# Kernel optimization log

Hardware: AMD Instinct MI355X
Metric: run time of the kernel (lower is better)

## Reference

```python
import jax, jax.numpy as jnp
import numpy as np

T = 64      # simulation_length
B = 128     # batch
D = 2048    # flattened input dim / axons per core
N = 2048    # neurons per core
L = 4       # number of cores (chain, latency = index)
OUT = 1024  # number of output_sources


def setup_inputs() -> dict:
    key = jax.random.key(0)
    k0, k1, k2, k3 = jax.random.split(key, 4)
    x = jax.random.uniform(k0, (B, D), dtype=jnp.float32)          # rate-coded input in [0,1)
    # core_params[l] = core_matrix.transpose() -> shape [N, A]; scaled for sane membrane dynamics
    W = jax.random.normal(k1, (L, N, D), dtype=jnp.float32) * 0.05
    thresholds = jnp.ones((L,), dtype=jnp.float32)
    # axon_sources: per-core irregular gather indices into previous core's neurons (input for l=0)
    axon_idx = jax.random.randint(k2, (L, D), 0, D, dtype=jnp.int32)
    out_idx = jax.random.randint(k3, (OUT,), 0, N, dtype=jnp.int32)
    return dict(x=x, W=W, thresholds=thresholds, axon_idx=axon_idx,
                out_idx=out_idx, simulation_length=T)


def _ideal_spike_scan(avg, thr, T):
    """Per-cycle: m += avg; spike = (m > thr); m[m > thr] -= thr.  avg: [B, N]."""
    def step(m, _):
        m = m + avg
        s = (m > thr).astype(m.dtype)
        return m - thr * s, s
    _, spikes = jax.lax.scan(step, jnp.zeros_like(avg), None, length=T)
    return spikes  # [T, B, N]


def reference(x, W, thresholds, axon_idx, out_idx, simulation_length):
    T = simulation_length
    L = W.shape[0]
    # generate_input_spike_train: x replicated across all cycles -> cache[-1]
    prev = jnp.broadcast_to(x, (T,) + x.shape)  # [T, B, D]
    for l in range(L):
        # get_signal_tensor: gather axon source signals for every cycle
        gathered = prev[:, :, axon_idx[l]]                    # [T, B, A]
        # per-cycle matmul: torch.matmul(core_params, sig.T).T == sig @ W[l].T
        val = jnp.einsum('tba,na->tbn', gathered, W[l])       # [T, B, N]
        avg = val.mean(axis=0)                                # avg_values [B, N]
        # ideal membrane integrate + threshold-reset recurrence -> out spike train
        prev = _ideal_spike_scan(avg, thresholds[l], T)       # [T, B, N]
    # output_signals: sum of output-source spikes over all cycles
    return prev[:, :, out_idx].sum(axis=0)                    # [B, OUT]
```

## Files before the change

kernel.cpp:

```cpp
#include <hip/hip_runtime.h>

#define BB   128
#define DD   2048
#define NN   2048
#define LL   4
#define OUTN 1024
#define JBQ  32
#define NDIG 5

#define NWDIG 12288
#define NG0   1024
#define NCSR  4

typedef double double4v __attribute__((ext_vector_type(4)));
typedef int    int4v    __attribute__((ext_vector_type(4)));
typedef char   char4v   __attribute__((ext_vector_type(4)));

__global__ __launch_bounds__(256) void prep_kernel(
    const float* __restrict__ W1,
    const float* __restrict__ x,
    const int*   __restrict__ axon,
    const int*   __restrict__ oidx,
    signed char* __restrict__ Wd,
    float*       __restrict__ At,
    int*         __restrict__ off,
    int*         __restrict__ lst)
{
    __shared__ int hist[2048];
    __shared__ int part[256];

    const int t  = threadIdx.x;
    const int bk = blockIdx.x;
    const size_t DP = (size_t)NN * DD;

    if (bk < NWDIG) {
        size_t i  = (size_t)bk * 256 + t;
        int    l  = (int)(i / (DP / 4));
        size_t e4 = i - (size_t)l * (DP / 4);
        int n = (int)(e4 >> 9);
        int k = (int)(e4 & 511) * 4;
        float4 w = *(const float4*)(W1 + (size_t)l * DP + (size_t)n * DD + k);
        const float wv[4] = {w.x, w.y, w.z, w.w};
        unsigned long long V[4];
        #pragma unroll
        for (int e = 0; e < 4; ++e)
            V[e] = (unsigned long long)(__double2ll_rn((double)wv[e] * 0x1p33)
                                        + (1LL << 34));
        signed char* base = Wd + (size_t)l * 5 * DP
                          + (size_t)(n >> 5) * 65536 + (size_t)(k >> 6) * 2048
                          + (n & 31) * 64 + (k & 63);
        #pragma unroll
        for (int j = 0; j < NDIG; ++j) {
            char4v p = { (char)((V[0] >> (7 * j)) & 127),
                         (char)((V[1] >> (7 * j)) & 127),
                         (char)((V[2] >> (7 * j)) & 127),
                         (char)((V[3] >> (7 * j)) & 127) };
            *(char4v*)(base + (size_t)j * DP) = p;
        }
        return;
    }
    if (bk < NWDIG + NG0) {
        int i = (bk - NWDIG) * 256 + t;
        int k = i >> 7;
        int b = i & 127;
        At[i] = x[b * DD + axon[k]];
        return;
    }
    {
        const int m   = bk - (NWDIG + NG0);
        const int* ip = (m < 3) ? (axon + (size_t)(m + 1) * DD) : oidx;
        const int cnt = (m < 3) ? DD : OUTN;
        int* offG = off + m * 2052;
        int* lstG = lst + m * 2048;

        for (int i = t; i < 2048; i += 256) hist[i] = 0;
        __syncthreads();
        for (int e = t; e < cnt; e += 256) atomicAdd(&hist[ip[e]], 1);
        __syncthreads();

        const int b0 = t * 8;
        int s = 0;
        #pragma unroll
        for (int i = 0; i < 8; ++i) s += hist[b0 + i];
        part[t] = s;
        __syncthreads();
        for (int d = 1; d < 256; d <<= 1) {
            int v = (t >= d) ? part[t - d] : 0;
            __syncthreads();
            part[t] += v;
            __syncthreads();
        }
        int base = part[t] - s;
        #pragma unroll
        for (int i = 0; i < 8; ++i) {
            int h = hist[b0 + i];
            offG[b0 + i] = base;
            hist[b0 + i] = base;
            base += h;
        }
        if (t == 255) offG[2048] = base;
        __syncthreads();
        for (int e = t; e < cnt; e += 256) {
            int n = ip[e];
            int pos = atomicAdd(&hist[n], 1);
            lstG[pos] = e;
        }
    }
}

__global__ __launch_bounds__(256, 2) void layer_kernel(
    const float* __restrict__ src,
    const int*   __restrict__ idx,
    int sR, int sB,
    const float* __restrict__ Wl,
    const float* __restrict__ thresholds, int l,
    const int*   __restrict__ Tptr,
    float* __restrict__ dst,
    const int* __restrict__ goff, const int* __restrict__ glst,
    signed char* __restrict__ g8n,
    const int* __restrict__ ooff, const int* __restrict__ olst,
    float* __restrict__ outp,
    int isLast)
{
    __shared__ double red[4 * 64 * 8];

    const int t    = threadIdx.x;
    const int wq   = t >> 6;
    const int lane = t & 63;
    const int q    = lane >> 4;
    const int c    = lane & 15;

    const int g     = blockIdx.x;
    const int btile = (g >> 3) & 7;
    const int nsup  = (g & 7) | ((g >> 6) << 3);
    const int n0    = nsup * 32;
    const int bcol  = btile * 16 + c;
    const size_t bo = (size_t)bcol * sB;

    double4v pr = {0., 0., 0., 0.}, pcv = {0., 0., 0., 0.};
    pr  = __builtin_amdgcn_mfma_f64_16x16x4f64(0.25 * (double)c, 1.0, pr, 0, 0, 0);
    pcv = __builtin_amdgcn_mfma_f64_16x16x4f64(0.25, (double)c, pcv, 0, 0, 0);
    int rowD[4], colD[4];
    #pragma unroll
    for (int r = 0; r < 4; ++r) {
        rowD[r] = (int)(pr[r] + 0.25);
        colD[r] = (int)(pcv[r] + 0.25);
    }

    double4v acc0[4] = {{0.,0.,0.,0.},{0.,0.,0.,0.},{0.,0.,0.,0.},{0.,0.,0.,0.}};
    double4v acc1[4] = {{0.,0.,0.,0.},{0.,0.,0.,0.},{0.,0.,0.,0.},{0.,0.,0.,0.}};

    const int    kbase = wq * (DD / 4);
    const float* wb0   = Wl + (size_t)(n0 + c) * DD + kbase + 4 * q;
    const float* wb1   = wb0 + (size_t)16 * DD;
    const int*   ibase = idx ? (idx + kbase + 4 * q) : nullptr;

    float4 wv0[4], wv1[4];
    float4 sv[4];
    int4   iv[4];

    #pragma unroll
    for (int p = 0; p < 4; ++p) {
        wv0[p] = *(const float4*)(wb0 + 16 * p);
        wv1[p] = *(const float4*)(wb1 + 16 * p);
    }
    #pragma unroll
    for (int p = 0; p < 4; ++p) {
        int r0, r1, r2, r3;
        if (ibase) {
            int4 iv0 = *(const int4*)(ibase + 16 * p);
            r0 = iv0.x; r1 = iv0.y; r2 = iv0.z; r3 = iv0.w;
        } else {
            int kb = kbase + 16 * p + 4 * q;
            r0 = kb; r1 = kb + 1; r2 = kb + 2; r3 = kb + 3;
        }
        sv[p].x = src[(size_t)r0 * sR + bo];
        sv[p].y = src[(size_t)r1 * sR + bo];
        sv[p].z = src[(size_t)r2 * sR + bo];
        sv[p].w = src[(size_t)r3 * sR + bo];
    }
    if (ibase) {
        #pragma unroll
        for (int p = 0; p < 4; ++p) iv[p] = *(const int4*)(ibase + 16 * (4 + p));
    }

    for (int u = 0; u < JBQ / 4; ++u) {
        #pragma unroll
        for (int gg = 0; gg < 4; ++gg) {
            float4 w0 = wv0[gg];
            float4 w1 = wv1[gg];
            float4 s  = sv[gg];

            int jn = 4 * u + 4 + gg; if (jn > JBQ - 1) jn = JBQ - 1;
            wv0[gg] = *(const float4*)(wb0 + 16 * jn);
            wv1[gg] = *(const float4*)(wb1 + 16 * jn);

            int r0, r1, r2, r3;
            if (ibase) {
                int4 ivv = iv[gg];
                r0 = ivv.x; r1 = ivv.y; r2 = ivv.z; r3 = ivv.w;
            } else {
                int kb = kbase + 16 * jn + 4 * q;
                r0 = kb; r1 = kb + 1; r2 = kb + 2; r3 = kb + 3;
            }
            sv[gg].x = src[(size_t)r0 * sR + bo];
            sv[gg].y = src[(size_t)r1 * sR + bo];
            sv[gg].z = src[(size_t)r2 * sR + bo];
            sv[gg].w = src[(size_t)r3 * sR + bo];

            if (ibase) {
                int jm = 4 * u + 8 + gg; if (jm > JBQ - 1) jm = JBQ - 1;
                iv[gg] = *(const int4*)(ibase + 16 * jm);
            }

            acc0[0] = __builtin_amdgcn_mfma_f64_16x16x4f64((double)w0.x, (double)s.x, acc0[0], 0, 0, 0);
            acc1[0] = __builtin_amdgcn_mfma_f64_16x16x4f64((double)w1.x, (double)s.x, acc1[0], 0, 0, 0);
            acc0[1] = __builtin_amdgcn_mfma_f64_16x16x4f64((double)w0.y, (double)s.y, acc0[1], 0, 0, 0);
            acc1[1] = __builtin_amdgcn_mfma_f64_16x16x4f64((double)w1.y, (double)s.y, acc1[1], 0, 0, 0);
            acc0[2] = __builtin_amdgcn_mfma_f64_16x16x4f64((double)w0.z, (double)s.z, acc0[2], 0, 0, 0);
            acc1[2] = __builtin_amdgcn_mfma_f64_16x16x4f64((double)w1.z, (double)s.z, acc1[2], 0, 0, 0);
            acc0[3] = __builtin_amdgcn_mfma_f64_16x16x4f64((double)w0.w, (double)s.w, acc0[3], 0, 0, 0);
            acc1[3] = __builtin_amdgcn_mfma_f64_16x16x4f64((double)w1.w, (double)s.w, acc1[3], 0, 0, 0);
        }
    }

    double4v a0 = (acc0[0] + acc0[1]) + (acc0[2] + acc0[3]);
    double4v a1 = (acc1[0] + acc1[1]) + (acc1[2] + acc1[3]);

    {
        double* my = red + ((size_t)wq * 64 + lane) * 8;
        #pragma unroll
        for (int r = 0; r < 4; ++r) { my[r] = a0[r]; my[4 + r] = a1[r]; }
    }
    __syncthreads();
    if (wq < 2) {
        const int off = wq * 4;
        double a[4];
        #pragma unroll
        for (int r = 0; r < 4; ++r) {
            a[r] =  red[((size_t)0 * 64 + lane) * 8 + off + r];
            a[r] += red[((size_t)1 * 64 + lane) * 8 + off + r];
            a[r] += red[((size_t)2 * 64 + lane) * 8 + off + r];
            a[r] += red[((size_t)3 * 64 + lane) * 8 + off + r];
        }

        const double th = (double)thresholds[l];
        const int T = *Tptr;
        const float sc = isLast ? 1.0f : (1.0f / (float)T);
        double m0 = 0., m1 = 0., m2 = 0., m3 = 0.;
        int c0 = 0, c1 = 0, c2 = 0, c3 = 0;
        for (int tt = 0; tt < T; ++tt) {
            m0 += a[0]; if (m0 > th) { c0++; m0 -= th; }
            m1 += a[1]; if (m1 > th) { c1++; m1 -= th; }
            m2 += a[2]; if (m2 > th) { c2++; m2 -= th; }
            m3 += a[3]; if (m3 > th) { c3++; m3 -= th; }
        }
        int cnt[4] = {c0, c1, c2, c3};
        #pragma unroll
        for (int r = 0; r < 4; ++r) {
            int n = n0 + 16 * wq + rowD[r];
            int b = btile * 16 + colD[r];
            if (dst)  dst[(size_t)n * BB + b] = (float)cnt[r] * sc;
            if (goff) {
                for (int j = goff[n]; j < goff[n + 1]; ++j) {
                    int k = glst[j];
                    g8n[(size_t)(k >> 6) * 8192 + b * 64 + (k & 63)] =
                        (signed char)cnt[r];
                }
            }
            if (ooff) {
                for (int j = ooff[n]; j < ooff[n + 1]; ++j)
                    outp[(size_t)b * OUTN + olst[j]] = (float)cnt[r];
            }
        }
    }
}

__global__ __launch_bounds__(256, 2) void layer_i8_kernel(
    const signed char* __restrict__ B8,
    const signed char* __restrict__ Wd5,
    const float* __restrict__ thresholds, int l,
    const int*   __restrict__ Tptr,
    const int* __restrict__ goff, const int* __restrict__ glst,
    signed char* __restrict__ g8n,
    const int* __restrict__ ooff, const int* __restrict__ olst,
    float* __restrict__ outp,
    int isLast)
{
    __shared__ double red[4 * 64 * 8];

    const int t    = threadIdx.x;
    const int wq   = t >> 6;
    const int lane = t & 63;
    const int q    = lane >> 4;
    const int c    = lane & 15;

    const int g     = blockIdx.x;
    const int btile = (g >> 3) & 7;
    const int nsup  = (g & 7) | ((g >> 6) << 3);
    const int n0    = nsup * 32;
    const int bcol  = btile * 16 + c;

    int rowD[4], colD[4];
    {
        const int cb  = c * 0x01010101;
        const int hot = (q == 0) ? 1 : 0;
        int4v aLab = {cb, cb, cb, cb};
        int4v oneh = {hot, 0, 0, 0};
        int4v dR = {0, 0, 0, 0}, dC = {0, 0, 0, 0};
        dR = __builtin_amdgcn_mfma_i32_16x16x64_i8(aLab, oneh, dR, 0, 0, 0);
        dC = __builtin_amdgcn_mfma_i32_16x16x64_i8(oneh, aLab, dC, 0, 0, 0);
        #pragma unroll
        for (int r = 0; r < 4; ++r) { rowD[r] = dR[r]; colD[r] = dC[r]; }
    }

    int4v acc0[NDIG], acc1[NDIG], accS = (int4v)0;
    #pragma unroll
    for (int j = 0; j < NDIG; ++j) { acc0[j] = (int4v)0; acc1[j] = (int4v)0; }

    const size_t DP = (size_t)NN * DD;
    const signed char* ab = Wd5 + (size_t)nsup * 65536 + c * 64 + q * 16;
    const signed char* bb = B8 + bcol * 64 + q * 16;

    const int4v ones = {0x01010101, 0x01010101, 0x01010101, 0x01010101};
    const int ck0 = wq * 8;

    int4v A0[NDIG], A1[NDIG], Bv;
    int4v N0[NDIG], N1[NDIG], Nb;

    {
        const signed char* ap = ab + (size_t)ck0 * 2048;
        #pragma unroll
        for (int j = 0; j < NDIG; ++j) {
            A0[j] = *(const int4v*)(ap + (size_t)j * DP);
            A1[j] = *(const int4v*)(ap + (size_t)j * DP + 1024);
        }
        Bv = *(const int4v*)(bb + (size_t)ck0 * 8192);
    }

    #pragma unroll 1
    for (int u = 0; u < 3; ++u) {
        {
            const signed char* ap = ab + (size_t)(ck0 + 2 * u + 1) * 2048;
            #pragma unroll
            for (int j = 0; j < NDIG; ++j) {
                N0[j] = *(const int4v*)(ap + (size_t)j * DP);
                N1[j] = *(const int4v*)(ap + (size_t)j * DP + 1024);
            }
            Nb = *(const int4v*)(bb + (size_t)(ck0 + 2 * u + 1) * 8192);
        }
        #pragma unroll
        for (int j = 0; j < NDIG; ++j) {
            acc0[j] = __builtin_amdgcn_mfma_i32_16x16x64_i8(A0[j], Bv, acc0[j], 0, 0, 0);
            acc1[j] = __builtin_amdgcn_mfma_i32_16x16x64_i8(A1[j], Bv, acc1[j], 0, 0, 0);
        }
        accS = __builtin_amdgcn_mfma_i32_16x16x64_i8(ones, Bv, accS, 0, 0, 0);
        {
            const signed char* ap = ab + (size_t)(ck0 + 2 * u + 2) * 2048;
            #pragma unroll
            for (int j = 0; j < NDIG; ++j) {
                A0[j] = *(const int4v*)(ap + (size_t)j * DP);
                A1[j] = *(const int4v*)(ap + (size_t)j * DP + 1024);
            }
            Bv = *(const int4v*)(bb + (size_t)(ck0 + 2 * u + 2) * 8192);
        }
        #pragma unroll
        for (int j = 0; j < NDIG; ++j) {
            acc0[j] = __builtin_amdgcn_mfma_i32_16x16x64_i8(N0[j], Nb, acc0[j], 0, 0, 0);
            acc1[j] = __builtin_amdgcn_mfma_i32_16x16x64_i8(N1[j], Nb, acc1[j], 0, 0, 0);
        }
        accS = __builtin_amdgcn_mfma_i32_16x16x64_i8(ones, Nb, accS, 0, 0, 0);
    }
    {
        const signed char* ap = ab + (size_t)(ck0 + 7) * 2048;
        #pragma unroll
        for (int j = 0; j < NDIG; ++j) {
            N0[j] = *(const int4v*)(ap + (size_t)j * DP);
            N1[j] = *(const int4v*)(ap + (size_t)j * DP + 1024);
        }
        Nb = *(const int4v*)(bb + (size_t)(ck0 + 7) * 8192);
    }
    #pragma unroll
    for (int j = 0; j < NDIG; ++j) {
        acc0[j] = __builtin_amdgcn_mfma_i32_16x16x64_i8(A0[j], Bv, acc0[j], 0, 0, 0);
        acc1[j] = __builtin_amdgcn_mfma_i32_16x16x64_i8(A1[j], Bv, acc1[j], 0, 0, 0);
    }
    accS = __builtin_amdgcn_mfma_i32_16x16x64_i8(ones, Bv, accS, 0, 0, 0);
    #pragma unroll
    for (int j = 0; j < NDIG; ++j) {
        acc0[j] = __builtin_amdgcn_mfma_i32_16x16x64_i8(N0[j], Nb, acc0[j], 0, 0, 0);
        acc1[j] = __builtin_amdgcn_mfma_i32_16x16x64_i8(N1[j], Nb, acc1[j], 0, 0, 0);
    }
    accS = __builtin_amdgcn_mfma_i32_16x16x64_i8(ones, Nb, accS, 0, 0, 0);

    const double S0 = 0x1p-33, S1 = 0x1p-26, S2 = 0x1p-19,
                 S3 = 0x1p-12, S4 = 0x1p-5;
    {
        double* my = red + ((size_t)wq * 64 + lane) * 8;
        #pragma unroll
        for (int r = 0; r < 4; ++r) {
            double corr = 2.0 * (double)accS[r];
            my[r]     = S0 * (double)acc0[0][r] + S1 * (double)acc0[1][r]
                      + S2 * (double)acc0[2][r] + S3 * (double)acc0[3][r]
                      + S4 * (double)acc0[4][r] - corr;
            my[4 + r] = S0 * (double)acc1[0][r] + S1 * (double)acc1[1][r]
                      + S2 * (double)acc1[2][r] + S3 * (double)acc1[3][r]
                      + S4 * (double)acc1[4][r] - corr;
        }
    }
    __syncthreads();
    if (wq < 2) {
        const int off = wq * 4;
        double a[4];
        #pragma unroll
        for (int r = 0; r < 4; ++r) {
            a[r] =  red[((size_t)0 * 64 + lane) * 8 + off + r];
            a[r] += red[((size_t)1 * 64 + lane) * 8 + off + r];
            a[r] += red[((size_t)2 * 64 + lane) * 8 + off + r];
            a[r] += red[((size_t)3 * 64 + lane) * 8 + off + r];
        }

        const double th = (double)thresholds[l];
        const int T = *Tptr;
        const double invT = 1.0 / (double)T;
        double m0 = 0., m1 = 0., m2 = 0., m3 = 0.;
        int c0 = 0, c1 = 0, c2 = 0, c3 = 0;
        const double v0 = a[0] * invT, v1 = a[1] * invT,
                     v2 = a[2] * invT, v3 = a[3] * invT;
        for (int tt = 0; tt < T; ++tt) {
            m0 += v0; if (m0 > th) { c0++; m0 -= th; }
            m1 += v1; if (m1 > th) { c1++; m1 -= th; }
            m2 += v2; if (m2 > th) { c2++; m2 -= th; }
            m3 += v3; if (m3 > th) { c3++; m3 -= th; }
        }
        int cnt[4] = {c0, c1, c2, c3};
        #pragma unroll
        for (int r = 0; r < 4; ++r) {
            int n = n0 + 16 * wq + rowD[r];
            int b = btile * 16 + colD[r];
            if (goff) {
                for (int j = goff[n]; j < goff[n + 1]; ++j) {
                    int k = glst[j];
                    g8n[(size_t)(k >> 6) * 8192 + b * 64 + (k & 63)] =
                        (signed char)cnt[r];
                }
            }
            if (ooff) {
                for (int j = ooff[n]; j < ooff[n + 1]; ++j)
                    outp[(size_t)b * OUTN + olst[j]] = (float)cnt[r];
            }
        }
    }
}

__global__ __launch_bounds__(256) void out_kernel(
    const float* __restrict__ cntT, const int* __restrict__ out_idx,
    float* __restrict__ out)
{
    int i = blockIdx.x * 256 + threadIdx.x;
    int b = i >> 10;
    int o = i & 1023;
    out[i] = cntT[(size_t)out_idx[o] * BB + b];
}

extern "C" void kernel_launch(void* const* d_in, const int* in_sizes, int n_in,
                              void* d_out, int out_size, void* d_ws, size_t ws_size,
                              hipStream_t stream)
{
    const float* x    = (const float*)d_in[0];
    const float* W    = (const float*)d_in[1];
    const float* thr  = (const float*)d_in[2];
    const int*   axon = (const int*)d_in[3];
    const int*   oidx = (const int*)d_in[4];
    const int*   Tptr = (const int*)d_in[5];
    float* out = (float*)d_out;

    const size_t DP = (size_t)NN * DD;
    char* ws = (char*)d_ws;
    float* At   = (float*)ws;
    float* mA   = (float*)(ws + (1u << 20));
    float* mB   = (float*)(ws + (2u << 20));
    float* cntT = (float*)(ws + (3u << 20));
    signed char* g8A = (signed char*)(ws + (4u << 20));
    signed char* g8B = (signed char*)(ws + (4u << 20) + (256u << 10));
    int* off = (int*)(ws + (4u << 20) + (512u << 10));
    int* lst = (int*)(ws + (4u << 20) + (640u << 10));
    signed char* Wd  = (signed char*)(ws + (5u << 20));

    const int useI8 = (ws_size >= ((size_t)80 << 20)) ? 1 : 0;

    if (!useI8) {
        const float* srcs[LL] = { x, mA, mB, mA };
        float*       dsts[LL] = { mA, mB, mA, cntT };
        for (int l = 0; l < LL; ++l) {
            layer_kernel<<<512, 256, 0, stream>>>(
                srcs[l], axon + (size_t)l * DD,
                (l == 0) ? 1 : BB, (l == 0) ? DD : 1,
                W + (size_t)l * NN * DD, thr, l, Tptr,
                dsts[l], nullptr, nullptr, nullptr, nullptr, nullptr, nullptr,
                (l == LL - 1) ? 1 : 0);
        }
        out_kernel<<<(BB * OUTN) / 256, 256, 0, stream>>>(cntT, oidx, out);
        return;
    }

    prep_kernel<<<NWDIG + NG0 + NCSR, 256, 0, stream>>>(
        W + DP, x, axon, oidx, Wd, At, off, lst);

    layer_kernel<<<512, 256, 0, stream>>>(
        At, nullptr, BB, 1, W, thr, 0, Tptr,
        nullptr, off + 0 * 2052, lst + 0 * 2048, g8A,
        nullptr, nullptr, nullptr, 0);

    layer_i8_kernel<<<512, 256, 0, stream>>>(
        g8A, Wd + 0 * 5 * DP, thr, 1, Tptr,
        off + 1 * 2052, lst + 1 * 2048, g8B,
        nullptr, nullptr, nullptr, 0);
    layer_i8_kernel<<<512, 256, 0, stream>>>(
        g8B, Wd + 1 * 5 * DP, thr, 2, Tptr,
        off + 2 * 2052, lst + 2 * 2048, g8A,
        nullptr, nullptr, nullptr, 0);
    layer_i8_kernel<<<512, 256, 0, stream>>>(
        g8A, Wd + 2 * 5 * DP, thr, 3, Tptr,
        nullptr, nullptr, nullptr,
        off + 3 * 2052, lst + 3 * 2048, out, 1);
}
```

Before: 215.1 us.

## Halve neuron tile per block and double grid for layer kernels, retile layer-0 input

Layer-0 now runs in a dedicated kernel with a 16-neuron tile, and its gathered input is stored in a k-chunked tiled layout that matches the int8 buffers. The int8 layer kernels also drop from 32 to 16 neurons per block, with the grid doubled to 1024 blocks and launch bounds raised to 4 blocks per CU. The aim is more parallelism and occupancy on the many CUs. In exchange, the software-pipelined double-buffered prefetch in the int8 kernel becomes a simple load-then-MFMA loop, and each block reuses its B operand over fewer neurons.

```diff
diff --git a/kernel.cpp b/kernel.cpp
--- a/kernel.cpp
+++ b/kernel.cpp
@@ -61,9 +61,9 @@
     }
     if (bk < NWDIG + NG0) {
         int i = (bk - NWDIG) * 256 + t;
-        int k = i >> 7;
-        int b = i & 127;
-        At[i] = x[b * DD + axon[k]];
+        int b = i >> 11;
+        int k = i & (DD - 1);
+        At[(size_t)(k >> 6) * 8192 + b * 64 + (k & 63)] = x[b * DD + axon[k]];
         return;
     }
     {
@@ -108,6 +108,231 @@
     }
 }
 
+__global__ __launch_bounds__(256, 4) void layer0_kernel(
+    const float* __restrict__ Atile,
+    const float* __restrict__ Wl,
+    const float* __restrict__ thr,
+    const int*   __restrict__ Tptr,
+    const int* __restrict__ goff, const int* __restrict__ glst,
+    signed char* __restrict__ g8n)
+{
+    __shared__ double red[4 * 64 * 4];
+
+    const int t    = threadIdx.x;
+    const int wq   = t >> 6;
+    const int lane = t & 63;
+    const int q    = lane >> 4;
+    const int c    = lane & 15;
+
+    const int g     = blockIdx.x;
+    const int btile = (g >> 3) & 7;
+    const int nsup  = (g & 7) | ((g >> 6) << 3);
+    const int n0    = nsup * 16;
+    const int bcol  = btile * 16 + c;
+
+    double4v pr = {0., 0., 0., 0.}, pcv = {0., 0., 0., 0.};
+    pr  = __builtin_amdgcn_mfma_f64_16x16x4f64(0.25 * (double)c, 1.0, pr, 0, 0, 0);
+    pcv = __builtin_amdgcn_mfma_f64_16x16x4f64(0.25, (double)c, pcv, 0, 0, 0);
+    int rowD[4], colD[4];
+    #pragma unroll
+    for (int r = 0; r < 4; ++r) {
+        rowD[r] = (int)(pr[r] + 0.25);
+        colD[r] = (int)(pcv[r] + 0.25);
+    }
+
+    double4v acc[4] = {{0.,0.,0.,0.},{0.,0.,0.,0.},{0.,0.,0.,0.},{0.,0.,0.,0.}};
+
+    const int    kbase = wq * (DD / 4);
+    const float* wb0   = Wl + (size_t)(n0 + c) * DD + kbase + 4 * q;
+
+    float4 wv0[4], sv[4];
+    #pragma unroll
+    for (int p = 0; p < 4; ++p) wv0[p] = *(const float4*)(wb0 + 16 * p);
+    #pragma unroll
+    for (int p = 0; p < 4; ++p) {
+        int kabs = kbase + 16 * p + 4 * q;
+        sv[p] = *(const float4*)(Atile + (size_t)(kabs >> 6) * 8192
+                                 + bcol * 64 + (kabs & 63));
+    }
+
+    for (int u = 0; u < JBQ / 4; ++u) {
+        #pragma unroll
+        for (int gg = 0; gg < 4; ++gg) {
+            float4 w0 = wv0[gg];
+            float4 s  = sv[gg];
+
+            int jn = 4 * u + 4 + gg; if (jn > JBQ - 1) jn = JBQ - 1;
+            wv0[gg] = *(const float4*)(wb0 + 16 * jn);
+            int kabs = kbase + 16 * jn + 4 * q;
+            sv[gg] = *(const float4*)(Atile + (size_t)(kabs >> 6) * 8192
+                                      + bcol * 64 + (kabs & 63));
+
+            acc[0] = __builtin_amdgcn_mfma_f64_16x16x4f64((double)w0.x, (double)s.x, acc[0], 0, 0, 0);
+            acc[1] = __builtin_amdgcn_mfma_f64_16x16x4f64((double)w0.y, (double)s.y, acc[1], 0, 0, 0);
+            acc[2] = __builtin_amdgcn_mfma_f64_16x16x4f64((double)w0.z, (double)s.z, acc[2], 0, 0, 0);
+            acc[3] = __builtin_amdgcn_mfma_f64_16x16x4f64((double)w0.w, (double)s.w, acc[3], 0, 0, 0);
+        }
+    }
+
+    double4v a0 = (acc[0] + acc[1]) + (acc[2] + acc[3]);
+    {
+        double* my = red + ((size_t)wq * 64 + lane) * 4;
+        #pragma unroll
+        for (int r = 0; r < 4; ++r) my[r] = a0[r];
+    }
+    __syncthreads();
+    if (wq == 0) {
+        double a[4];
+        #pragma unroll
+        for (int r = 0; r < 4; ++r) {
+            a[r] =  red[((size_t)0 * 64 + lane) * 4 + r];
+            a[r] += red[((size_t)1 * 64 + lane) * 4 + r];
+            a[r] += red[((size_t)2 * 64 + lane) * 4 + r];
+            a[r] += red[((size_t)3 * 64 + lane) * 4 + r];
+        }
+
+        const double th = (double)thr[0];
+        const int T = *Tptr;
+        double m0 = 0., m1 = 0., m2 = 0., m3 = 0.;
+        int c0 = 0, c1 = 0, c2 = 0, c3 = 0;
+        for (int tt = 0; tt < T; ++tt) {
+            m0 += a[0]; if (m0 > th) { c0++; m0 -= th; }
+            m1 += a[1]; if (m1 > th) { c1++; m1 -= th; }
+            m2 += a[2]; if (m2 > th) { c2++; m2 -= th; }
+            m3 += a[3]; if (m3 > th) { c3++; m3 -= th; }
+        }
+        int cnt[4] = {c0, c1, c2, c3};
+        #pragma unroll
+        for (int r = 0; r < 4; ++r) {
+            int n = n0 + rowD[r];
+            int b = btile * 16 + colD[r];
+            for (int j = goff[n]; j < goff[n + 1]; ++j) {
+                int k = glst[j];
+                g8n[(size_t)(k >> 6) * 8192 + b * 64 + (k & 63)] =
+                    (signed char)cnt[r];
+            }
+        }
+    }
+}
+
+__global__ __launch_bounds__(256, 4) void layer_i8_kernel(
+    const signed char* __restrict__ B8,
+    const signed char* __restrict__ Wd5,
+    const float* __restrict__ thr, int l,
+    const int*   __restrict__ Tptr,
+    const int* __restrict__ goff, const int* __restrict__ glst,
+    signed char* __restrict__ g8n,
+    const int* __restrict__ ooff, const int* __restrict__ olst,
+    float* __restrict__ outp)
+{
+    __shared__ double red[4 * 64 * 4];
+
+    const int t    = threadIdx.x;
+    const int wq   = t >> 6;
+    const int lane = t & 63;
+    const int q    = lane >> 4;
+    const int c    = lane & 15;
+
+    const int g     = blockIdx.x;
+    const int btile = (g >> 3) & 7;
+    const int nsup  = (g & 7) | ((g >> 6) << 3);
+    const int n0    = nsup * 16;
+    const int bcol  = btile * 16 + c;
+
+    int rowD[4], colD[4];
+    {
+        const int cb  = c * 0x01010101;
+        const int hot = (q == 0) ? 1 : 0;
+        int4v aLab = {cb, cb, cb, cb};
+        int4v oneh = {hot, 0, 0, 0};
+        int4v dR = {0, 0, 0, 0}, dC = {0, 0, 0, 0};
+        dR = __builtin_amdgcn_mfma_i32_16x16x64_i8(aLab, oneh, dR, 0, 0, 0);
+        dC = __builtin_amdgcn_mfma_i32_16x16x64_i8(oneh, aLab, dC, 0, 0, 0);
+        #pragma unroll
+        for (int r = 0; r < 4; ++r) { rowD[r] = dR[r]; colD[r] = dC[r]; }
+    }
+
+    int4v acc[NDIG], accS = (int4v)0;
+    #pragma unroll
+    for (int j = 0; j < NDIG; ++j) acc[j] = (int4v)0;
+
+    const size_t DP = (size_t)NN * DD;
+    const signed char* ab = Wd5 + (size_t)(nsup >> 1) * 65536
+                          + (nsup & 1) * 1024 + c * 64 + q * 16;
+    const signed char* bb = B8 + bcol * 64 + q * 16;
+
+    const int4v ones = {0x01010101, 0x01010101, 0x01010101, 0x01010101};
+    const int ck0 = wq * 8;
+
+    #pragma unroll 1
+    for (int kc = 0; kc < 8; ++kc) {
+        const signed char* ap = ab + (size_t)(ck0 + kc) * 2048;
+        int4v A[NDIG], Bv;
+        #pragma unroll
+        for (int j = 0; j < NDIG; ++j)
+            A[j] = *(const int4v*)(ap + (size_t)j * DP);
+        Bv = *(const int4v*)(bb + (size_t)(ck0 + kc) * 8192);
+        #pragma unroll
+        for (int j = 0; j < NDIG; ++j)
+            acc[j] = __builtin_amdgcn_mfma_i32_16x16x64_i8(A[j], Bv, acc[j], 0, 0, 0);
+        accS = __builtin_amdgcn_mfma_i32_16x16x64_i8(ones, Bv, accS, 0, 0, 0);
+    }
+
+    const double S0 = 0x1p-33, S1 = 0x1p-26, S2 = 0x1p-19,
+                 S3 = 0x1p-12, S4 = 0x1p-5;
+    {
+        double* my = red + ((size_t)wq * 64 + lane) * 4;
+        #pragma unroll
+        for (int r = 0; r < 4; ++r) {
+            my[r] = S0 * (double)acc[0][r] + S1 * (double)acc[1][r]
+                  + S2 * (double)acc[2][r] + S3 * (double)acc[3][r]
+                  + S4 * (double)acc[4][r] - 2.0 * (double)accS[r];
+        }
+    }
+    __syncthreads();
+    if (wq == 0) {
+        double a[4];
+        #pragma unroll
+        for (int r = 0; r < 4; ++r) {
+            a[r] =  red[((size_t)0 * 64 + lane) * 4 + r];
+            a[r] += red[((size_t)1 * 64 + lane) * 4 + r];
+            a[r] += red[((size_t)2 * 64 + lane) * 4 + r];
+            a[r] += red[((size_t)3 * 64 + lane) * 4 + r];
+        }
+
+        const double th = (double)thr[l];
+        const int T = *Tptr;
+        const double invT = 1.0 / (double)T;
+        double m0 = 0., m1 = 0., m2 = 0., m3 = 0.;
+        int c0 = 0, c1 = 0, c2 = 0, c3 = 0;
+        const double v0 = a[0] * invT, v1 = a[1] * invT,
+                     v2 = a[2] * invT, v3 = a[3] * invT;
+        for (int tt = 0; tt < T; ++tt) {
+            m0 += v0; if (m0 > th) { c0++; m0 -= th; }
+            m1 += v1; if (m1 > th) { c1++; m1 -= th; }
+            m2 += v2; if (m2 > th) { c2++; m2 -= th; }
+            m3 += v3; if (m3 > th) { c3++; m3 -= th; }
+        }
+        int cnt[4] = {c0, c1, c2, c3};
+        #pragma unroll
+        for (int r = 0; r < 4; ++r) {
+            int n = n0 + rowD[r];
+            int b = btile * 16 + colD[r];
+            if (goff) {
+                for (int j = goff[n]; j < goff[n + 1]; ++j) {
+                    int k = glst[j];
+                    g8n[(size_t)(k >> 6) * 8192 + b * 64 + (k & 63)] =
+                        (signed char)cnt[r];
+                }
+            }
+            if (ooff) {
+                for (int j = ooff[n]; j < ooff[n + 1]; ++j)
+                    outp[(size_t)b * OUTN + olst[j]] = (float)cnt[r];
+            }
+        }
+    }
+}
+
 __global__ __launch_bounds__(256, 2) void layer_kernel(
     const float* __restrict__ src,
     const int*   __restrict__ idx,
@@ -115,12 +340,7 @@
     const float* __restrict__ Wl,
     const float* __restrict__ thresholds, int l,
     const int*   __restrict__ Tptr,
-    float* __restrict__ dst,
-    const int* __restrict__ goff, const int* __restrict__ glst,
-    signed char* __restrict__ g8n,
-    const int* __restrict__ ooff, const int* __restrict__ olst,
-    float* __restrict__ outp,
-    int isLast)
+    float* __restrict__ dst, int isLast)
 {
     __shared__ double red[4 * 64 * 8];
 
@@ -260,195 +480,7 @@
         for (int r = 0; r < 4; ++r) {
             int n = n0 + 16 * wq + rowD[r];
             int b = btile * 16 + colD[r];
-            if (dst)  dst[(size_t)n * BB + b] = (float)cnt[r] * sc;
-            if (goff) {
-                for (int j = goff[n]; j < goff[n + 1]; ++j) {
-                    int k = glst[j];
-                    g8n[(size_t)(k >> 6) * 8192 + b * 64 + (k & 63)] =
-                        (signed char)cnt[r];
-                }
-            }
-            if (ooff) {
-                for (int j = ooff[n]; j < ooff[n + 1]; ++j)
-                    outp[(size_t)b * OUTN + olst[j]] = (float)cnt[r];
-            }
-        }
-    }
-}
-
-__global__ __launch_bounds__(256, 2) void layer_i8_kernel(
-    const signed char* __restrict__ B8,
-    const signed char* __restrict__ Wd5,
-    const float* __restrict__ thresholds, int l,
-    const int*   __restrict__ Tptr,
-    const int* __restrict__ goff, const int* __restrict__ glst,
-    signed char* __restrict__ g8n,
-    const int* __restrict__ ooff, const int* __restrict__ olst,
-    float* __restrict__ outp,
-    int isLast)
-{
-    __shared__ double red[4 * 64 * 8];
-
-    const int t    = threadIdx.x;
-    const int wq   = t >> 6;
-    const int lane = t & 63;
-    const int q    = lane >> 4;
-    const int c    = lane & 15;
-
-    const int g     = blockIdx.x;
-    const int btile = (g >> 3) & 7;
-    const int nsup  = (g & 7) | ((g >> 6) << 3);
-    const int n0    = nsup * 32;
-    const int bcol  = btile * 16 + c;
-
-    int rowD[4], colD[4];
-    {
-        const int cb  = c * 0x01010101;
-        const int hot = (q == 0) ? 1 : 0;
-        int4v aLab = {cb, cb, cb, cb};
-        int4v oneh = {hot, 0, 0, 0};
-        int4v dR = {0, 0, 0, 0}, dC = {0, 0, 0, 0};
-        dR = __builtin_amdgcn_mfma_i32_16x16x64_i8(aLab, oneh, dR, 0, 0, 0);
-        dC = __builtin_amdgcn_mfma_i32_16x16x64_i8(oneh, aLab, dC, 0, 0, 0);
-        #pragma unroll
-        for (int r = 0; r < 4; ++r) { rowD[r] = dR[r]; colD[r] = dC[r]; }
-    }
-
-    int4v acc0[NDIG], acc1[NDIG], accS = (int4v)0;
-    #pragma unroll
-    for (int j = 0; j < NDIG; ++j) { acc0[j] = (int4v)0; acc1[j] = (int4v)0; }
-
-    const size_t DP = (size_t)NN * DD;
-    const signed char* ab = Wd5 + (size_t)nsup * 65536 + c * 64 + q * 16;
-    const signed char* bb = B8 + bcol * 64 + q * 16;
-
-    const int4v ones = {0x01010101, 0x01010101, 0x01010101, 0x01010101};
-    const int ck0 = wq * 8;
-
-    int4v A0[NDIG], A1[NDIG], Bv;
-    int4v N0[NDIG], N1[NDIG], Nb;
-
-    {
-        const signed char* ap = ab + (size_t)ck0 * 2048;
-        #pragma unroll
-        for (int j = 0; j < NDIG; ++j) {
-            A0[j] = *(const int4v*)(ap + (size_t)j * DP);
-            A1[j] = *(const int4v*)(ap + (size_t)j * DP + 1024);
-        }
-        Bv = *(const int4v*)(bb + (size_t)ck0 * 8192);
-    }
-
-    #pragma unroll 1
-    for (int u = 0; u < 3; ++u) {
-        {
-            const signed char* ap = ab + (size_t)(ck0 + 2 * u + 1) * 2048;
-            #pragma unroll
-            for (int j = 0; j < NDIG; ++j) {
-                N0[j] = *(const int4v*)(ap + (size_t)j * DP);
-                N1[j] = *(const int4v*)(ap + (size_t)j * DP + 1024);
-            }
-            Nb = *(const int4v*)(bb + (size_t)(ck0 + 2 * u + 1) * 8192);
-        }
-        #pragma unroll
-        for (int j = 0; j < NDIG; ++j) {
-            acc0[j] = __builtin_amdgcn_mfma_i32_16x16x64_i8(A0[j], Bv, acc0[j], 0, 0, 0);
-            acc1[j] = __builtin_amdgcn_mfma_i32_16x16x64_i8(A1[j], Bv, acc1[j], 0, 0, 0);
-        }
-        accS = __builtin_amdgcn_mfma_i32_16x16x64_i8(ones, Bv, accS, 0, 0, 0);
-        {
-            const signed char* ap = ab + (size_t)(ck0 + 2 * u + 2) * 2048;
-            #pragma unroll
-            for (int j = 0; j < NDIG; ++j) {
-                A0[j] = *(const int4v*)(ap + (size_t)j * DP);
-                A1[j] = *(const int4v*)(ap + (size_t)j * DP + 1024);
-            }
-            Bv = *(const int4v*)(bb + (size_t)(ck0 + 2 * u + 2) * 8192);
-        }
-        #pragma unroll
-        for (int j = 0; j < NDIG; ++j) {
-            acc0[j] = __builtin_amdgcn_mfma_i32_16x16x64_i8(N0[j], Nb, acc0[j], 0, 0, 0);
-            acc1[j] = __builtin_amdgcn_mfma_i32_16x16x64_i8(N1[j], Nb, acc1[j], 0, 0, 0);
-        }
-        accS = __builtin_amdgcn_mfma_i32_16x16x64_i8(ones, Nb, accS, 0, 0, 0);
-    }
-    {
-        const signed char* ap = ab + (size_t)(ck0 + 7) * 2048;
-        #pragma unroll
-        for (int j = 0; j < NDIG; ++j) {
-            N0[j] = *(const int4v*)(ap + (size_t)j * DP);
-            N1[j] = *(const int4v*)(ap + (size_t)j * DP + 1024);
-        }
-        Nb = *(const int4v*)(bb + (size_t)(ck0 + 7) * 8192);
-    }
-    #pragma unroll
-    for (int j = 0; j < NDIG; ++j) {
-        acc0[j] = __builtin_amdgcn_mfma_i32_16x16x64_i8(A0[j], Bv, acc0[j], 0, 0, 0);
-        acc1[j] = __builtin_amdgcn_mfma_i32_16x16x64_i8(A1[j], Bv, acc1[j], 0, 0, 0);
-    }
-    accS = __builtin_amdgcn_mfma_i32_16x16x64_i8(ones, Bv, accS, 0, 0, 0);
-    #pragma unroll
-    for (int j = 0; j < NDIG; ++j) {
-        acc0[j] = __builtin_amdgcn_mfma_i32_16x16x64_i8(N0[j], Nb, acc0[j], 0, 0, 0);
-        acc1[j] = __builtin_amdgcn_mfma_i32_16x16x64_i8(N1[j], Nb, acc1[j], 0, 0, 0);
-    }
-    accS = __builtin_amdgcn_mfma_i32_16x16x64_i8(ones, Nb, accS, 0, 0, 0);
-
-    const double S0 = 0x1p-33, S1 = 0x1p-26, S2 = 0x1p-19,
-                 S3 = 0x1p-12, S4 = 0x1p-5;
-    {
-        double* my = red + ((size_t)wq * 64 + lane) * 8;
-        #pragma unroll
-        for (int r = 0; r < 4; ++r) {
-            double corr = 2.0 * (double)accS[r];
-            my[r]     = S0 * (double)acc0[0][r] + S1 * (double)acc0[1][r]
-                      + S2 * (double)acc0[2][r] + S3 * (double)acc0[3][r]
-                      + S4 * (double)acc0[4][r] - corr;
-            my[4 + r] = S0 * (double)acc1[0][r] + S1 * (double)acc1[1][r]
-                      + S2 * (double)acc1[2][r] + S3 * (double)acc1[3][r]
-                      + S4 * (double)acc1[4][r] - corr;
-        }
-    }
-    __syncthreads();
-    if (wq < 2) {
-        const int off = wq * 4;
-        double a[4];
-        #pragma unroll
-        for (int r = 0; r < 4; ++r) {
-            a[r] =  red[((size_t)0 * 64 + lane) * 8 + off + r];
-            a[r] += red[((size_t)1 * 64 + lane) * 8 + off + r];
-            a[r] += red[((size_t)2 * 64 + lane) * 8 + off + r];
-            a[r] += red[((size_t)3 * 64 + lane) * 8 + off + r];
-        }
-
-        const double th = (double)thresholds[l];
-        const int T = *Tptr;
-        const double invT = 1.0 / (double)T;
-        double m0 = 0., m1 = 0., m2 = 0., m3 = 0.;
-        int c0 = 0, c1 = 0, c2 = 0, c3 = 0;
-        const double v0 = a[0] * invT, v1 = a[1] * invT,
-                     v2 = a[2] * invT, v3 = a[3] * invT;
-        for (int tt = 0; tt < T; ++tt) {
-            m0 += v0; if (m0 > th) { c0++; m0 -= th; }
-            m1 += v1; if (m1 > th) { c1++; m1 -= th; }
-            m2 += v2; if (m2 > th) { c2++; m2 -= th; }
-            m3 += v3; if (m3 > th) { c3++; m3 -= th; }
-        }
-        int cnt[4] = {c0, c1, c2, c3};
-        #pragma unroll
-        for (int r = 0; r < 4; ++r) {
-            int n = n0 + 16 * wq + rowD[r];
-            int b = btile * 16 + colD[r];
-            if (goff) {
-                for (int j = goff[n]; j < goff[n + 1]; ++j) {
-                    int k = glst[j];
-                    g8n[(size_t)(k >> 6) * 8192 + b * 64 + (k & 63)] =
-                        (signed char)cnt[r];
-                }
-            }
-            if (ooff) {
-                for (int j = ooff[n]; j < ooff[n + 1]; ++j)
-                    outp[(size_t)b * OUTN + olst[j]] = (float)cnt[r];
-            }
+            dst[(size_t)n * BB + b] = (float)cnt[r] * sc;
         }
     }
 }
@@ -497,8 +529,7 @@
                 srcs[l], axon + (size_t)l * DD,
                 (l == 0) ? 1 : BB, (l == 0) ? DD : 1,
                 W + (size_t)l * NN * DD, thr, l, Tptr,
-                dsts[l], nullptr, nullptr, nullptr, nullptr, nullptr, nullptr,
-                (l == LL - 1) ? 1 : 0);
+                dsts[l], (l == LL - 1) ? 1 : 0);
         }
         out_kernel<<<(BB * OUTN) / 256, 256, 0, stream>>>(cntT, oidx, out);
         return;
@@ -507,21 +538,19 @@
     prep_kernel<<<NWDIG + NG0 + NCSR, 256, 0, stream>>>(
         W + DP, x, axon, oidx, Wd, At, off, lst);
 
-    layer_kernel<<<512, 256, 0, stream>>>(
-        At, nullptr, BB, 1, W, thr, 0, Tptr,
-        nullptr, off + 0 * 2052, lst + 0 * 2048, g8A,
-        nullptr, nullptr, nullptr, 0);
-
-    layer_i8_kernel<<<512, 256, 0, stream>>>(
+    layer0_kernel<<<1024, 256, 0, stream>>>(
+        At, W, thr, Tptr, off + 0 * 2052, lst + 0 * 2048, g8A);
+
+    layer_i8_kernel<<<1024, 256, 0, stream>>>(
         g8A, Wd + 0 * 5 * DP, thr, 1, Tptr,
         off + 1 * 2052, lst + 1 * 2048, g8B,
-        nullptr, nullptr, nullptr, 0);
-    layer_i8_kernel<<<512, 256, 0, stream>>>(
+        nullptr, nullptr, nullptr);
+    layer_i8_kernel<<<1024, 256, 0, stream>>>(
         g8B, Wd + 1 * 5 * DP, thr, 2, Tptr,
         off + 2 * 2052, lst + 2 * 2048, g8A,
-        nullptr, nullptr, nullptr, 0);
-    layer_i8_kernel<<<512, 256, 0, stream>>>(
+        nullptr, nullptr, nullptr);
+    layer_i8_kernel<<<1024, 256, 0, stream>>>(
         g8A, Wd + 2 * 5 * DP, thr, 3, Tptr,
         nullptr, nullptr, nullptr,
-        off + 3 * 2052, lst + 3 * 2048, out, 1);
+        off + 3 * 2052, lst + 3 * 2048, out);
 }
```

Result: no change. 218.2 us (+1.5%).
